# Kernel optimization log

Hardware: AMD Instinct MI355X
Metric: run time of the kernel (lower is better)

Reference implementation:

```python
import jax, jax.numpy as jnp
import numpy as np

B = 1
T_FRAMES = 512
LDIM = 512
D = 512
H = 8
DH = 64
L = 8
FF = 2048
CTX = 250
RATIOS = (8, 6, 5, 4)
MAX_PERIOD = 10000.0


def setup_inputs() -> dict:
    key = jax.random.key(0)
    ks = iter(jax.random.split(key, 80))
    def rn(shape, s=0.02):
        return jax.random.normal(next(ks), shape, jnp.float32) * s
    inp = {}
    inp['latent'] = rn((B, LDIM, T_FRAMES), 1.0)
    inp['emb_std'] = jax.random.uniform(next(ks), (LDIM,), jnp.float32, 0.5, 1.5)
    inp['emb_mean'] = rn((LDIM,), 0.1)
    inp['quant_w'] = rn((D, LDIM)); inp['quant_b'] = jnp.zeros((D,))
    inp['up_w'] = rn((D, D, 4)); inp['up_b'] = jnp.zeros((D,))
    inp['n1w'] = jnp.ones((L, D)); inp['n1b'] = jnp.zeros((L, D))
    inp['ipw'] = rn((L, 3 * D, D)); inp['ipb'] = jnp.zeros((L, 3 * D))
    inp['opw'] = rn((L, D, D)); inp['opb'] = jnp.zeros((L, D))
    inp['ls1'] = jnp.full((L, D), 0.01)
    inp['n2w'] = jnp.ones((L, D)); inp['n2b'] = jnp.zeros((L, D))
    inp['l1w'] = rn((L, FF, D)); inp['l1b'] = jnp.zeros((L, FF))
    inp['l2w'] = rn((L, D, FF)); inp['l2b'] = jnp.zeros((L, D))
    inp['ls2'] = jnp.full((L, D), 0.01)
    inp['tproj_w'] = rn((D, D)); inp['tproj_b'] = jnp.zeros((D,))
    inp['dc0_w'] = rn((1024, D, 7)); inp['dc0_b'] = jnp.zeros((1024,))
    ch = 1024
    for i, r in enumerate(RATIOS, 1):
        co = ch // 2
        inp['t%d_w' % i] = rn((ch, co, 2 * r)); inp['t%d_b' % i] = jnp.zeros((co,))
        inp['r%da_w' % i] = rn((co // 2, co, 3)); inp['r%da_b' % i] = jnp.zeros((co // 2,))
        inp['r%db_w' % i] = rn((co, co // 2, 1)); inp['r%db_b' % i] = jnp.zeros((co,))
        ch = co
    inp['df_w'] = rn((1, 64, 7)); inp['df_b'] = jnp.zeros((1,))
    return {k: jnp.asarray(v, jnp.float32) for k, v in inp.items()}


def _ln(x, w, b):
    m = x.mean(-1, keepdims=True)
    v = ((x - m) ** 2).mean(-1, keepdims=True)
    return (x - m) / jnp.sqrt(v + 1e-5) * w + b


def _rope(x, cos, sin):
    # x: (B,T,H,DH); cos/sin: (T,1,DH//2)
    b_, t_, h_, d_ = x.shape
    xr = x.reshape(b_, t_, h_, d_ // 2, 2)
    re, im = xr[..., 0], xr[..., 1]
    out = jnp.stack([re * cos - im * sin, re * sin + im * cos], axis=-1)
    return out.reshape(b_, t_, h_, d_)


def _conv(x, w, b, stride=1):
    # StreamingConv1d non-streaming: left-pad by k-stride (zeros), then valid conv.
    k = w.shape[-1]
    pad = k - stride
    if pad > 0:
        x = jnp.pad(x, ((0, 0), (0, 0), (pad, 0)))
    y = jax.lax.conv_general_dilated(x, w, (stride,), 'VALID',
                                     dimension_numbers=('NCH', 'OIH', 'NCH'))
    return y + b[None, :, None]


def _convtr(x, w, b, stride):
    # torch ConvTranspose1d, padding=0: w is (in, out, k); L_out=(L-1)*stride+k
    k = w.shape[-1]
    w2 = jnp.swapaxes(jnp.flip(w, -1), 0, 1)  # (out, in, k)
    y = jax.lax.conv_general_dilated(x, w2, (1,), [(k - 1, k - 1)],
                                     lhs_dilation=(stride,),
                                     dimension_numbers=('NCH', 'OIH', 'NCH'))
    return y + b[None, :, None]


def _forward(latent, emb_std, emb_mean, quant_w, quant_b, up_w, up_b,
             n1w, n1b, ipw, ipb, opw, opb, ls1, n2w, n2b, l1w, l1b, l2w, l2b, ls2,
             tproj_w, tproj_b, dc0_w, dc0_b,
             t1_w, t1_b, r1a_w, r1a_b, r1b_w, r1b_b,
             t2_w, t2_b, r2a_w, r2a_b, r2b_w, r2b_b,
             t3_w, t3_b, r3a_w, r3a_b, r3b_w, r3b_b,
             t4_w, t4_b, r4a_w, r4a_b, r4b_w, r4b_b,
             df_w, df_b):
    # denormalize + quantizer output proj (1x1 conv)
    x = latent * emb_std[None, :, None] + emb_mean[None, :, None]
    x = jnp.einsum('od,bdt->bot', quant_w, x) + quant_b[None, :, None]
    # upsample (raw convtr, no trimming)
    x = _convtr(x, up_w, up_b, 2)
    z = jnp.swapaxes(x, 1, 2)  # (B, T, D)
    T = z.shape[1]
    # windowed causal additive mask: attend to previous `CTX` positions incl. self
    pos = jnp.arange(T)
    delta = pos[:, None] - pos[None, :]
    mask = jnp.where((delta >= 0) & (delta < CTX), 0.0, -jnp.inf).astype(jnp.float32)
    # RoPE tables (offset = 0)
    fr = jnp.exp(jnp.arange(DH // 2, dtype=jnp.float32) * (-np.log(MAX_PERIOD) * 2.0 / DH))
    ang = jnp.arange(T, dtype=jnp.float32)[:, None, None] * fr  # (T,1,DH//2)
    cos, sin = jnp.cos(ang), jnp.sin(ang)
    scale = 1.0 / np.sqrt(DH)

    def step(h, p):
        n1w_, n1b_, ipw_, ipb_, opw_, opb_, ls1_, n2w_, n2b_, l1w_, l1b_, l2w_, l2b_, ls2_ = p
        hn = _ln(h, n1w_, n1b_)
        qkv = (jnp.einsum('btd,ed->bte', hn, ipw_) + ipb_).reshape(B, T, 3, H, DH)
        q, k, v = qkv[:, :, 0], qkv[:, :, 1], qkv[:, :, 2]
        q = _rope(q, cos, sin)
        k = _rope(k, cos, sin)
        s = jnp.einsum('bqhd,bkhd->bhqk', q, k) * scale + mask
        a = jax.nn.softmax(s, axis=-1)
        o = jnp.einsum('bhqk,bkhd->bqhd', a, v).reshape(B, T, D)
        o = jnp.einsum('btd,ed->bte', o, opw_) + opb_
        h = h + ls1_ * o
        hn2 = _ln(h, n2w_, n2b_)
        ff = jax.nn.gelu(jnp.einsum('btd,fd->btf', hn2, l1w_) + l1b_, approximate=False)
        ff = jnp.einsum('btf,df->btd', ff, l2w_) + l2b_
        h = h + ls2_ * ff
        return h, None

    z, _ = jax.lax.scan(step, z, (n1w, n1b, ipw, ipb, opw, opb, ls1,
                                  n2w, n2b, l1w, l1b, l2w, l2b, ls2))
    z = jnp.einsum('btd,ed->bte', z, tproj_w) + tproj_b
    z = jnp.swapaxes(z, 1, 2)  # (B, D, T)
    # SEANet decoder
    z = _conv(z, dc0_w, dc0_b, 1)
    stages = ((t1_w, t1_b, r1a_w, r1a_b, r1b_w, r1b_b, 8),
              (t2_w, t2_b, r2a_w, r2a_b, r2b_w, r2b_b, 6),
              (t3_w, t3_b, r3a_w, r3a_b, r3b_w, r3b_b, 5),
              (t4_w, t4_b, r4a_w, r4a_b, r4b_w, r4b_b, 4))
    for tw, tb, raw_, rab_, rbw_, rbb_, st in stages:
        z = jax.nn.elu(z)
        z = _convtr(z, tw, tb, st)
        v2 = _conv(jax.nn.elu(z), raw_, rab_, 1)
        v2 = _conv(jax.nn.elu(v2), rbw_, rbb_, 1)
        z = z + v2  # residual block skip
    z = jax.nn.elu(z)
    z = _conv(z, df_w, df_b, 1)
    return z  # (B, 1, T_samples)


def reference(latent, emb_std, emb_mean, quant_w, quant_b, up_w, up_b,
              n1w, n1b, ipw, ipb, opw, opb, ls1, n2w, n2b, l1w, l1b, l2w, l2b, ls2,
              tproj_w, tproj_b, dc0_w, dc0_b,
              t1_w, t1_b, r1a_w, r1a_b, r1b_w, r1b_b,
              t2_w, t2_b, r2a_w, r2a_b, r2b_w, r2b_b,
              t3_w, t3_b, r3a_w, r3a_b, r3b_w, r3b_b,
              t4_w, t4_b, r4a_w, r4a_b, r4b_w, r4b_b,
              df_w, df_b):
    return _forward(latent, emb_std, emb_mean, quant_w, quant_b, up_w, up_b,
                    n1w, n1b, ipw, ipb, opw, opb, ls1, n2w, n2b, l1w, l1b, l2w, l2b, ls2,
                    tproj_w, tproj_b, dc0_w, dc0_b,
                    t1_w, t1_b, r1a_w, r1a_b, r1b_w, r1b_b,
                    t2_w, t2_b, r2a_w, r2a_b, r2b_w, r2b_b,
                    t3_w, t3_b, r3a_w, r3a_b, r3b_w, r3b_b,
                    t4_w, t4_b, r4a_w, r4a_b, r4b_w, r4b_b,
                    df_w, df_b)
```

## Files before the change

kernel.cpp:

```cpp
#include <hip/hip_runtime.h>
#include <math.h>

typedef __attribute__((ext_vector_type(8))) short short8;
typedef __attribute__((ext_vector_type(4))) float f32x4;

#define MFMA16(a, b, c) __builtin_amdgcn_mfma_f32_16x16x32_bf16((a), (b), (c), 0, 0, 0)

__device__ __forceinline__ unsigned bfu(float f) {
    unsigned u = __float_as_uint(f);
    return (u + 0x7fffu + ((u >> 16) & 1u)) >> 16;
}

static constexpr int TT   = 1026;
static constexpr int T_S1 = 8216;
static constexpr int T_S2 = 49302;
static constexpr int T_S3 = 246515;
static constexpr int T_S4 = 986064;

static constexpr int NCH    = 8;
static constexpr int LC     = T_S4 / NCH;
static constexpr int LE_MAX = LC + 8;

static constexpr size_t O_X0  = 0;
static constexpr size_t O_XQ  = 262144;
static constexpr size_t O_XU  = 524288;
static constexpr size_t O_Z   = 1049600;
static constexpr size_t O_HN  = 1574912;
static constexpr size_t O_QKV = 2100224;
static constexpr size_t O_AO  = 3676160;
static constexpr size_t O_FF  = 4201472;
static constexpr size_t O_COS = 6302720;
static constexpr size_t O_SIN = 6335552;
static constexpr size_t O_ZT  = 6368384;
static constexpr size_t O_ZC  = 6893696;
static constexpr size_t O_D0  = 7419008;
static constexpr size_t O_Z1  = 8469632;
static constexpr size_t O_V1  = 12676224;
static constexpr size_t O_Z2  = 31553920;
static constexpr size_t O_V2  = 0;
static constexpr size_t O_Z3  = 0;
static constexpr size_t O_V3  = 31553920;
static constexpr size_t O_Z4C = 31553920;
static constexpr size_t O_VAC = 39442944;

static inline int cdiv(int a, int b) { return (a + b - 1) / b; }

__global__ __launch_bounds__(256) void embed_k(const float* __restrict__ lat,
    const float* __restrict__ sd, const float* __restrict__ mn, float* __restrict__ y)
{
    int i = blockIdx.x * 256 + threadIdx.x;
    if (i >= 512 * 512) return;
    int c = i >> 9;
    y[i] = lat[i] * sd[c] + mn[c];
}

__global__ __launch_bounds__(256) void rope_tables(float* __restrict__ cs, float* __restrict__ sn)
{
    int idx = blockIdx.x * 256 + threadIdx.x;
    if (idx >= TT * 32) return;
    int i = idx & 31;
    int t = idx >> 5;
    float fr = expf(-(float)i * (logf(10000.f) / 32.f));
    float ang = (float)t * fr;
    cs[idx] = cosf(ang);
    sn[idx] = sinf(ang);
}

__global__ __launch_bounds__(256) void rope_apply(float* __restrict__ qkv,
    const float* __restrict__ cs, const float* __restrict__ sn)
{
    int idx = blockIdx.x * 256 + threadIdx.x;
    if (idx >= TT * 8 * 32) return;
    int i = idx & 31;
    int h = (idx >> 5) & 7;
    int t = idx >> 8;
    float c = cs[t * 32 + i], s = sn[t * 32 + i];
    size_t base = (size_t)t * 1536 + h * 64 + 2 * i;
    float re = qkv[base], im = qkv[base + 1];
    qkv[base]     = re * c - im * s;
    qkv[base + 1] = re * s + im * c;
    base += 512;
    re = qkv[base]; im = qkv[base + 1];
    qkv[base]     = re * c - im * s;
    qkv[base + 1] = re * s + im * c;
}

__global__ __launch_bounds__(256) void transpose_k(const float* __restrict__ in,
    float* __restrict__ out, int R, int C)
{
    __shared__ float tile[32][33];
    int c0 = blockIdx.x * 32, r0 = blockIdx.y * 32;
    int tx = threadIdx.x & 31, ty = threadIdx.x >> 5;
    for (int dy = ty; dy < 32; dy += 8) {
        int r = r0 + dy, c = c0 + tx;
        tile[dy][tx] = (r < R && c < C) ? in[(size_t)r * C + c] : 0.f;
    }
    __syncthreads();
    for (int dy = ty; dy < 32; dy += 8) {
        int c = c0 + dy, r = r0 + tx;
        if (c < C && r < R) out[(size_t)c * R + r] = tile[tx][dy];
    }
}

__global__ __launch_bounds__(256) void ln_kernel(const float* __restrict__ x,
    const float* __restrict__ w, const float* __restrict__ b, float* __restrict__ y)
{
    int t = blockIdx.x, tid = threadIdx.x;
    const float* xr = x + (size_t)t * 512;
    float v0 = xr[tid], v1 = xr[tid + 256];
    float s = v0 + v1, q = v0 * v0 + v1 * v1;
    for (int off = 32; off; off >>= 1) {
        s += __shfl_down(s, off);
        q += __shfl_down(q, off);
    }
    __shared__ float ss[4], qq[4], mb[2];
    int wid = tid >> 6, lane = tid & 63;
    if (lane == 0) { ss[wid] = s; qq[wid] = q; }
    __syncthreads();
    if (tid == 0) {
        float S = ss[0] + ss[1] + ss[2] + ss[3];
        float Q = qq[0] + qq[1] + qq[2] + qq[3];
        float m = S * (1.f / 512.f);
        float var = Q * (1.f / 512.f) - m * m;
        mb[0] = m;
        mb[1] = rsqrtf(var + 1e-5f);
    }
    __syncthreads();
    float m = mb[0], inv = mb[1];
    y[(size_t)t * 512 + tid]       = (v0 - m) * inv * w[tid] + b[tid];
    y[(size_t)t * 512 + tid + 256] = (v1 - m) * inv * w[tid + 256] + b[tid + 256];
}

__global__ __launch_bounds__(256) void attn_kernel(const float* __restrict__ qkv,
    float* __restrict__ o)
{
    int t = blockIdx.x, h = blockIdx.y, tid = threadIdx.x;
    __shared__ float sq[64];
    __shared__ float sp[256];
    __shared__ float red[256];
    __shared__ float pacc[4][64];
    int klo = t - 249; if (klo < 0) klo = 0;
    int kc = t - klo + 1;
    if (tid < 64) sq[tid] = qkv[(size_t)t * 1536 + h * 64 + tid];
    __syncthreads();
    float sval = -3.0e38f;
    if (tid < kc) {
        const float* kr = qkv + (size_t)(klo + tid) * 1536 + 512 + h * 64;
        float d = 0.f;
#pragma unroll 8
        for (int i = 0; i < 64; i++) d += sq[i] * kr[i];
        sval = d * 0.125f;
    }
    red[tid] = sval;
    __syncthreads();
    for (int s2 = 128; s2 > 0; s2 >>= 1) {
        if (tid < s2) red[tid] = fmaxf(red[tid], red[tid + s2]);
        __syncthreads();
    }
    float m = red[0];
    __syncthreads();
    float p = (tid < kc) ? __expf(sval - m) : 0.f;
    sp[tid] = p;
    red[tid] = p;
    __syncthreads();
    for (int s2 = 128; s2 > 0; s2 >>= 1) {
        if (tid < s2) red[tid] += red[tid + s2];
        __syncthreads();
    }
    float inv = 1.f / red[0];
    int d = tid & 63, g = tid >> 6;
    float a = 0.f;
#pragma unroll 4
    for (int kk = g; kk < kc; kk += 4)
        a += sp[kk] * qkv[(size_t)(klo + kk) * 1536 + 1024 + h * 64 + d];
    pacc[g][d] = a;
    __syncthreads();
    if (tid < 64) {
        float r = (pacc[0][tid] + pacc[1][tid] + pacc[2][tid] + pacc[3][tid]) * inv;
        o[(size_t)t * 512 + h * 64 + tid] = r;
    }
}

template <int EPI>
__global__ __launch_bounds__(256, 3) void mfma_gemm(const float* __restrict__ A,
    const float* __restrict__ Wt, const float* __restrict__ bias,
    const float* __restrict__ ls, float* __restrict__ C, int M, int N, int K)
{
    constexpr int STR = 72;
    __shared__ unsigned short sA[128 * STR];
    __shared__ unsigned short sB[128 * STR];
    int tid = threadIdx.x;
    int m0 = blockIdx.y * 128, n0 = blockIdx.x * 128;
    int w = tid >> 6, lane = tid & 63;
    int wm = (w >> 1) * 64, wn = (w & 1) * 64;
    int row15 = lane & 15, q8 = (lane >> 4) * 8;
    int rb = tid >> 3;
    int sg = (tid & 7) * 8;
    f32x4 acc[4][4] = {};
    float4 av[8], bv[8];
    const float4 z4 = make_float4(0.f, 0.f, 0.f, 0.f);
    for (int k0 = 0; k0 < K; k0 += 64) {
#pragma unroll
        for (int it = 0; it < 4; it++) {
            int r = rb + it * 32;
            int gm = m0 + r;
            if (gm < M) {
                const float4* p = (const float4*)(A + (size_t)gm * K + k0 + sg);
                av[2 * it] = p[0]; av[2 * it + 1] = p[1];
            } else { av[2 * it] = z4; av[2 * it + 1] = z4; }
            int gn = n0 + r;
            if (gn < N) {
                const float4* p = (const float4*)(Wt + (size_t)gn * K + k0 + sg);
                bv[2 * it] = p[0]; bv[2 * it + 1] = p[1];
            } else { bv[2 * it] = z4; bv[2 * it + 1] = z4; }
        }
        __syncthreads();
#pragma unroll
        for (int it = 0; it < 4; it++) {
            int r = rb + it * 32;
            unsigned* d = (unsigned*)&sA[r * STR + sg];
            float4 f0 = av[2 * it], f1 = av[2 * it + 1];
            d[0] = bfu(f0.x) | (bfu(f0.y) << 16); d[1] = bfu(f0.z) | (bfu(f0.w) << 16);
            d[2] = bfu(f1.x) | (bfu(f1.y) << 16); d[3] = bfu(f1.z) | (bfu(f1.w) << 16);
            d = (unsigned*)&sB[r * STR + sg];
            f0 = bv[2 * it]; f1 = bv[2 * it + 1];
            d[0] = bfu(f0.x) | (bfu(f0.y) << 16); d[1] = bfu(f0.z) | (bfu(f0.w) << 16);
            d[2] = bfu(f1.x) | (bfu(f1.y) << 16); d[3] = bfu(f1.z) | (bfu(f1.w) << 16);
        }
        __syncthreads();
#pragma unroll
        for (int kk = 0; kk < 64; kk += 32) {
            short8 af[4], bf[4];
#pragma unroll
            for (int f = 0; f < 4; f++) {
                af[f] = *(const short8*)&sA[(wm + f * 16 + row15) * STR + kk + q8];
                bf[f] = *(const short8*)&sB[(wn + f * 16 + row15) * STR + kk + q8];
            }
#pragma unroll
            for (int i = 0; i < 4; i++)
#pragma unroll
                for (int j = 0; j < 4; j++)
                    acc[i][j] = MFMA16(af[i], bf[j], acc[i][j]);
        }
    }
    int rq = (lane >> 4) * 4;
#pragma unroll
    for (int i = 0; i < 4; i++) {
#pragma unroll
        for (int r = 0; r < 4; r++) {
            int m = m0 + wm + i * 16 + rq + r;
            if (m >= M) continue;
#pragma unroll
            for (int j = 0; j < 4; j++) {
                int n = n0 + wn + j * 16 + row15;
                float v = acc[i][j][r] + bias[n];
                size_t idx = (size_t)m * N + n;
                if (EPI == 0) C[idx] = v;
                else if (EPI == 1) C[idx] = 0.5f * v * (1.f + erff(v * 0.70710678118654752f));
                else C[idx] += ls[n] * v;
            }
        }
    }
}

template <int K, bool ELU_IN, bool ACC>
__global__ __launch_bounds__(256, 3) void mfma_conv(
    const float* __restrict__ x, const float* __restrict__ w,
    const float* __restrict__ bias, float* __restrict__ y,
    int Ci, int Co, int x_str, int Tx, int x_t0, int Ty, int y_t0, int to_lo, int to_hi)
{
    constexpr int TL = 128 + K - 1;
    constexpr int SX = 40;
    constexpr int SW = 40;
    constexpr int NX = (32 * TL + 255) / 256;
    constexpr int NWK = 8 * K;
    __shared__ unsigned short sX[TL * SX];
    __shared__ unsigned short sW[K * 64 * SW];
    int tid = threadIdx.x;
    int co0 = blockIdx.y * 64;
    int t_base = to_lo + blockIdx.x * 128;
    int w_id = tid >> 6, lane = tid & 63;
    int wm = (w_id >> 1) * 32, wn = (w_id & 1) * 64;
    int row15 = lane & 15, q8 = (lane >> 4) * 8;
    f32x4 acc[2][4] = {};
    float xv[NX], wv[NWK];
    for (int ci0 = 0; ci0 < Ci; ci0 += 32) {
#pragma unroll
        for (int it = 0; it < NX; it++) {
            int i = tid + it * 256;
            float v = 0.f;
            if (i < 32 * TL) {
                int ci = i / TL, tl = i - ci * TL;
                int gl = t_base - (K - 1) + tl - x_t0;
                if (gl >= 0 && gl < Tx) v = x[(size_t)(ci0 + ci) * x_str + gl];
            }
            xv[it] = v;
        }
#pragma unroll
        for (int it = 0; it < NWK; it++) {
            int i = tid + it * 256;
            int co = i / (32 * K), r = i - co * (32 * K);
            int ci = r / K, j = r - ci * K;
            wv[it] = (co0 + co < Co)
                ? w[((size_t)(co0 + co) * Ci + ci0 + ci) * K + j] : 0.f;
        }
        __syncthreads();
#pragma unroll
        for (int it = 0; it < NX; it++) {
            int i = tid + it * 256;
            if (i < 32 * TL) {
                int ci = i / TL, tl = i - ci * TL;
                float v = xv[it];
                if (ELU_IN) v = v > 0.f ? v : __expf(v) - 1.f;
                sX[tl * SX + ci] = (unsigned short)bfu(v);
            }
        }
#pragma unroll
        for (int it = 0; it < NWK; it++) {
            int i = tid + it * 256;
            int co = i / (32 * K), r = i - co * (32 * K);
            int ci = r / K, j = r - ci * K;
            sW[(j * 64 + co) * SW + ci] = (unsigned short)bfu(wv[it]);
        }
        __syncthreads();
#pragma unroll
        for (int j = 0; j < K; j++) {
            short8 af[2], bf[4];
#pragma unroll
            for (int f = 0; f < 2; f++)
                af[f] = *(const short8*)&sW[(j * 64 + wm + f * 16 + row15) * SW + q8];
#pragma unroll
            for (int f = 0; f < 4; f++)
                bf[f] = *(const short8*)&sX[(wn + f * 16 + row15 + j) * SX + q8];
#pragma unroll
            for (int i = 0; i < 2; i++)
#pragma unroll
                for (int f = 0; f < 4; f++)
                    acc[i][f] = MFMA16(af[i], bf[f], acc[i][f]);
        }
    }
    int rq = (lane >> 4) * 4;
#pragma unroll
    for (int i = 0; i < 2; i++) {
#pragma unroll
        for (int r = 0; r < 4; r++) {
            int co = co0 + wm + i * 16 + rq + r;
            if (co >= Co) continue;
            float b = bias[co];
#pragma unroll
            for (int f = 0; f < 4; f++) {
                int t = t_base + wn + f * 16 + row15;
                if (t < to_hi) {
                    size_t idx = (size_t)co * Ty + (t - y_t0);
                    float v = acc[i][f][r] + b;
                    if (ACC) y[idx] += v; else y[idx] = v;
                }
            }
        }
    }
}

template <int S, int PG, bool ELU_IN>
__global__ __launch_bounds__(256, 3) void mfma_convtr(
    const float* __restrict__ x, const float* __restrict__ w,
    const float* __restrict__ bias, float* __restrict__ y,
    int Ci, int Co, int Ti, int Ty, int y_t0, int q_lo, int to_lo, int to_hi)
{
    constexpr int SX = 40;
    constexpr int SW = 40;
    constexpr int NW = PG * 2;
    __shared__ unsigned short sX[256 * SX];
    __shared__ unsigned short sW[PG * 16 * SW];
    int tid = threadIdx.x;
    int co0 = blockIdx.y * 16;
    int q0 = q_lo + blockIdx.x * 256;
    int p0 = blockIdx.z * PG;
    int w_id = tid >> 6, lane = tid & 63;
    int row15 = lane & 15, q8 = (lane >> 4) * 8;
    f32x4 acc[PG][4] = {};
    int q = q0 + tid;
    bool qok0 = (q >= 0) && (q < Ti);
    bool qok1 = (q >= 1) && (q <= Ti);
    float xv0[16], xv1[16], wv[NW];

    auto prefetch = [&](int ci0) {
#pragma unroll
        for (int it = 0; it < 16; it++) {
            const float* xr = x + (size_t)(ci0 + it) * Ti;
            xv0[it] = qok0 ? xr[q] : 0.f;
            xv1[it] = qok1 ? xr[q - 1] : 0.f;
        }
#pragma unroll
        for (int it = 0; it < NW; it++) {
            int i = tid + it * 256;
            int pl = i >> 9, r = i & 511;
            int co = r >> 5, k = r & 31;
            int ci = k >> 1, tap = k & 1;
            wv[it] = (p0 + pl < S)
                ? w[((size_t)(ci0 + ci) * Co + co0 + co) * (2 * S) + tap * S + p0 + pl]
                : 0.f;
        }
    };
    auto commit = [&]() {
#pragma unroll
        for (int it = 0; it < 16; it++) {
            float v0 = xv0[it], v1 = xv1[it];
            if (ELU_IN) {
                v0 = v0 > 0.f ? v0 : __expf(v0) - 1.f;
                v1 = v1 > 0.f ? v1 : __expf(v1) - 1.f;
            }
            *(unsigned*)&sX[tid * SX + 2 * it] = bfu(v0) | (bfu(v1) << 16);
        }
#pragma unroll
        for (int it = 0; it < NW; it++) {
            int i = tid + it * 256;
            int pl = i >> 9, r = i & 511;
            int co = r >> 5, k = r & 31;
            sW[(pl * 16 + co) * SW + k] = (unsigned short)bfu(wv[it]);
        }
    };

    prefetch(0);
    for (int ci0 = 0; ci0 < Ci; ci0 += 16) {
        __syncthreads();
        commit();
        if (ci0 + 16 < Ci) prefetch(ci0 + 16);
        __syncthreads();
        short8 bf[4];
#pragma unroll
        for (int f = 0; f < 4; f++)
            bf[f] = *(const short8*)&sX[(w_id * 64 + f * 16 + row15) * SX + q8];
#pragma unroll
        for (int p = 0; p < PG; p++) {
            short8 af = *(const short8*)&sW[(p * 16 + row15) * SW + q8];
#pragma unroll
            for (int f = 0; f < 4; f++)
                acc[p][f] = MFMA16(af, bf[f], acc[p][f]);
        }
    }
    int rq = (lane >> 4) * 4;
#pragma unroll
    for (int r = 0; r < 4; r++) {
        int co = co0 + rq + r;
        float b = bias[co];
#pragma unroll
        for (int f = 0; f < 4; f++) {
            int qq = q0 + w_id * 64 + f * 16 + row15;
#pragma unroll
            for (int p = 0; p < PG; p++) {
                int to = qq * S + p0 + p;
                if (to >= to_lo && to < to_hi)
                    y[(size_t)co * Ty + (to - y_t0)] = acc[p][f][r] + b;
            }
        }
    }
}

__global__ __launch_bounds__(256) void conv7_out_chunk(const float* __restrict__ z4c,
    const float* __restrict__ w, const float* __restrict__ bias,
    float* __restrict__ out, int ext0, int t0, int cnt)
{
    __shared__ float ws_w[64 * 7];
    int tl = blockIdx.x * 256 + threadIdx.x;
    for (int i = threadIdx.x; i < 448; i += 256) ws_w[i] = w[i];
    __syncthreads();
    if (tl >= cnt) return;
    int t = t0 + tl;
    float acc = bias[0];
    for (int ci = 0; ci < 64; ci++) {
        const float* xr = z4c + (size_t)ci * LE_MAX;
#pragma unroll
        for (int j = 0; j < 7; j++) {
            int tg = t - 6 + j;
            float v = 0.f;
            if (tg >= 0) {
                float z = xr[tg - ext0];
                v = z > 0.f ? z : __expf(z) - 1.f;
            }
            acc += ws_w[ci * 7 + j] * v;
        }
    }
    out[t] = acc;
}

template <int K, bool ELU_IN, bool ACC>
static void conv_launch(const float* x, const float* w, const float* b, float* y,
    int Ci, int Co, int x_str, int Tx, int x_t0, int Ty, int y_t0, int to_lo, int to_hi,
    hipStream_t stream)
{
    dim3 g(cdiv(to_hi - to_lo, 128), cdiv(Co, 64));
    mfma_conv<K, ELU_IN, ACC><<<g, 256, 0, stream>>>(x, w, b, y, Ci, Co, x_str, Tx, x_t0, Ty, y_t0, to_lo, to_hi);
}

template <int S, int PG, bool ELU_IN>
static void convtr_launch(const float* x, const float* w, const float* b, float* y,
    int Ci, int Co, int Ti, int Ty, int y_t0, int to_lo, int to_hi, hipStream_t stream)
{
    int q_lo = to_lo / S;
    int q_hi = (to_hi - 1) / S;
    dim3 g(cdiv(q_hi - q_lo + 1, 256), Co / 16, cdiv(S, PG));
    mfma_convtr<S, PG, ELU_IN><<<g, 256, 0, stream>>>(x, w, b, y, Ci, Co, Ti, Ty, y_t0, q_lo, to_lo, to_hi);
}

extern "C" void kernel_launch(void* const* d_in, const int* in_sizes, int n_in,
                              void* d_out, int out_size, void* d_ws, size_t ws_size,
                              hipStream_t stream)
{
    const float* latent  = (const float*)d_in[0];
    const float* emb_std = (const float*)d_in[1];
    const float* emb_mean= (const float*)d_in[2];
    const float* quant_w = (const float*)d_in[3];
    const float* quant_b = (const float*)d_in[4];
    const float* up_w    = (const float*)d_in[5];
    const float* up_b    = (const float*)d_in[6];
    const float* n1w     = (const float*)d_in[7];
    const float* n1b     = (const float*)d_in[8];
    const float* ipw     = (const float*)d_in[9];
    const float* ipb     = (const float*)d_in[10];
    const float* opw     = (const float*)d_in[11];
    const float* opb     = (const float*)d_in[12];
    const float* ls1     = (const float*)d_in[13];
    const float* n2w     = (const float*)d_in[14];
    const float* n2b     = (const float*)d_in[15];
    const float* l1w     = (const float*)d_in[16];
    const float* l1b     = (const float*)d_in[17];
    const float* l2w     = (const float*)d_in[18];
    const float* l2b     = (const float*)d_in[19];
    const float* ls2     = (const float*)d_in[20];
    const float* tproj_w = (const float*)d_in[21];
    const float* tproj_b = (const float*)d_in[22];
    const float* dc0_w   = (const float*)d_in[23];
    const float* dc0_b   = (const float*)d_in[24];
    const float* df_w    = (const float*)d_in[49];
    const float* df_b    = (const float*)d_in[50];

    float* W = (float*)d_ws;
    float* OUT = (float*)d_out;

    embed_k<<<cdiv(512 * 512, 256), 256, 0, stream>>>(latent, emb_std, emb_mean, W + O_X0);
    conv_launch<1, false, false>(W + O_X0, quant_w, quant_b, W + O_XQ,
        512, 512, 512, 512, 0, 512, 0, 0, 512, stream);
    convtr_launch<2, 2, false>(W + O_XQ, up_w, up_b, W + O_XU,
        512, 512, 512, TT, 0, 0, TT, stream);
    transpose_k<<<dim3(cdiv(TT, 32), cdiv(512, 32)), 256, 0, stream>>>(W + O_XU, W + O_Z, 512, TT);
    rope_tables<<<cdiv(TT * 32, 256), 256, 0, stream>>>(W + O_COS, W + O_SIN);

    for (int l = 0; l < 8; l++) {
        ln_kernel<<<TT, 256, 0, stream>>>(W + O_Z, n1w + l * 512, n1b + l * 512, W + O_HN);
        mfma_gemm<0><<<dim3(1536 / 128, cdiv(TT, 128)), 256, 0, stream>>>(
            W + O_HN, ipw + (size_t)l * 1536 * 512, ipb + l * 1536, nullptr, W + O_QKV, TT, 1536, 512);
        rope_apply<<<cdiv(TT * 8 * 32, 256), 256, 0, stream>>>(W + O_QKV, W + O_COS, W + O_SIN);
        attn_kernel<<<dim3(TT, 8), 256, 0, stream>>>(W + O_QKV, W + O_AO);
        mfma_gemm<2><<<dim3(512 / 128, cdiv(TT, 128)), 256, 0, stream>>>(
            W + O_AO, opw + (size_t)l * 512 * 512, opb + l * 512, ls1 + l * 512, W + O_Z, TT, 512, 512);
        ln_kernel<<<TT, 256, 0, stream>>>(W + O_Z, n2w + l * 512, n2b + l * 512, W + O_HN);
        mfma_gemm<1><<<dim3(2048 / 128, cdiv(TT, 128)), 256, 0, stream>>>(
            W + O_HN, l1w + (size_t)l * 2048 * 512, l1b + l * 2048, nullptr, W + O_FF, TT, 2048, 512);
        mfma_gemm<2><<<dim3(512 / 128, cdiv(TT, 128)), 256, 0, stream>>>(
            W + O_FF, l2w + (size_t)l * 512 * 2048, l2b + l * 512, ls2 + l * 512, W + O_Z, TT, 512, 2048);
    }

    mfma_gemm<0><<<dim3(512 / 128, cdiv(TT, 128)), 256, 0, stream>>>(
        W + O_Z, tproj_w, tproj_b, nullptr, W + O_ZT, TT, 512, 512);
    transpose_k<<<dim3(cdiv(512, 32), cdiv(TT, 32)), 256, 0, stream>>>(W + O_ZT, W + O_ZC, TT, 512);
    conv_launch<7, false, false>(W + O_ZC, dc0_w, dc0_b, W + O_D0,
        512, 1024, TT, TT, 0, TT, 0, 0, TT, stream);

    {
        const float* tw = (const float*)d_in[25]; const float* tb = (const float*)d_in[26];
        const float* raw = (const float*)d_in[27]; const float* rab = (const float*)d_in[28];
        const float* rbw = (const float*)d_in[29]; const float* rbb = (const float*)d_in[30];
        convtr_launch<8, 4, true>(W + O_D0, tw, tb, W + O_Z1,
            1024, 512, TT, T_S1, 0, 0, T_S1, stream);
        conv_launch<3, true, false>(W + O_Z1, raw, rab, W + O_V1,
            512, 256, T_S1, T_S1, 0, T_S1, 0, 0, T_S1, stream);
        conv_launch<1, true, true>(W + O_V1, rbw, rbb, W + O_Z1,
            256, 512, T_S1, T_S1, 0, T_S1, 0, 0, T_S1, stream);
    }
    {
        const float* tw = (const float*)d_in[31]; const float* tb = (const float*)d_in[32];
        const float* raw = (const float*)d_in[33]; const float* rab = (const float*)d_in[34];
        const float* rbw = (const float*)d_in[35]; const float* rbb = (const float*)d_in[36];
        convtr_launch<6, 3, true>(W + O_Z1, tw, tb, W + O_Z2,
            512, 256, T_S1, T_S2, 0, 0, T_S2, stream);
        conv_launch<3, true, false>(W + O_Z2, raw, rab, W + O_V2,
            256, 128, T_S2, T_S2, 0, T_S2, 0, 0, T_S2, stream);
        conv_launch<1, true, true>(W + O_V2, rbw, rbb, W + O_Z2,
            128, 256, T_S2, T_S2, 0, T_S2, 0, 0, T_S2, stream);
    }
    {
        const float* tw = (const float*)d_in[37]; const float* tb = (const float*)d_in[38];
        const float* raw = (const float*)d_in[39]; const float* rab = (const float*)d_in[40];
        const float* rbw = (const float*)d_in[41]; const float* rbb = (const float*)d_in[42];
        convtr_launch<5, 5, true>(W + O_Z2, tw, tb, W + O_Z3,
            256, 128, T_S2, T_S3, 0, 0, T_S3, stream);
        conv_launch<3, true, false>(W + O_Z3, raw, rab, W + O_V3,
            128, 64, T_S3, T_S3, 0, T_S3, 0, 0, T_S3, stream);
        conv_launch<1, true, true>(W + O_V3, rbw, rbb, W + O_Z3,
            64, 128, T_S3, T_S3, 0, T_S3, 0, 0, T_S3, stream);
    }
    {
        const float* tw = (const float*)d_in[43]; const float* tb = (const float*)d_in[44];
        const float* raw = (const float*)d_in[45]; const float* rab = (const float*)d_in[46];
        const float* rbw = (const float*)d_in[47]; const float* rbb = (const float*)d_in[48];
        for (int c = 0; c < NCH; c++) {
            int t0 = c * LC;
            int ext0 = (c == 0) ? 0 : t0 - 8;
            int Le = t0 + LC - ext0;
            int vlo = (c == 0) ? 0 : ext0 + 2;
            convtr_launch<4, 4, true>(W + O_Z3, tw, tb, W + O_Z4C,
                128, 64, T_S3, LE_MAX, ext0, ext0, ext0 + Le, stream);
            conv_launch<3, true, false>(W + O_Z4C, raw, rab, W + O_VAC,
                64, 32, LE_MAX, Le, ext0, LE_MAX, ext0, vlo, ext0 + Le, stream);
            conv_launch<1, true, true>(W + O_VAC, rbw, rbb, W + O_Z4C,
                32, 64, LE_MAX, Le, ext0, LE_MAX, ext0, vlo, ext0 + Le, stream);
            conv7_out_chunk<<<dim3(cdiv(LC, 256), 1), 256, 0, stream>>>(
                W + O_Z4C, df_w, df_b, OUT, ext0, t0, LC);
        }
    }
}
```

Measured before the change: 5.857 ms.

## Split-K with atomics for small convs, add prefetch pipelining and block swizzle

Adds a split-K mode over input channels to the conv and transposed-conv kernels. Partial sums are combined with atomicAdd into zero-filled outputs, which gives the small early layers enough blocks to fill the GPU. It also adds register prefetch of the next K-tile in the GEMM and conv loops, vectorised float4 weight loads in the conv, and a block-index swizzle meant to improve cache locality. The costs are extra zero-fill launches, atomic traffic, and non-deterministic float summation order.

```diff
diff --git a/kernel.cpp b/kernel.cpp
--- a/kernel.cpp
+++ b/kernel.cpp
@@ -9,6 +9,17 @@
 __device__ __forceinline__ unsigned bfu(float f) {
     unsigned u = __float_as_uint(f);
     return (u + 0x7fffu + ((u >> 16) & 1u)) >> 16;
+}
+
+__device__ __forceinline__ void swz_block(unsigned& bx, unsigned& by, unsigned& bz) {
+    unsigned gx = gridDim.x, gy = gridDim.y, gz = gridDim.z;
+    unsigned nb = gx * gy * gz;
+    unsigned d = blockIdx.x + gx * (blockIdx.y + gy * blockIdx.z);
+    if ((nb & 7u) == 0u) d = (d & 7u) * (nb >> 3) + (d >> 3);
+    bx = d % gx;
+    unsigned r = d / gx;
+    by = r % gy;
+    bz = r / gy;
 }
 
 static constexpr int TT   = 1026;
@@ -45,6 +56,18 @@
 
 static inline int cdiv(int a, int b) { return (a + b - 1) / b; }
 
+__global__ __launch_bounds__(256) void fill0(float4* __restrict__ p, int n4)
+{
+    int i = blockIdx.x * 256 + threadIdx.x;
+    if (i < n4) p[i] = make_float4(0.f, 0.f, 0.f, 0.f);
+}
+
+static void zero_launch(float* p, size_t n, hipStream_t s)
+{
+    int n4 = (int)(n / 4);
+    fill0<<<cdiv(n4, 256), 256, 0, s>>>((float4*)p, n4);
+}
+
 __global__ __launch_bounds__(256) void embed_k(const float* __restrict__ lat,
     const float* __restrict__ sd, const float* __restrict__ mn, float* __restrict__ y)
 {
@@ -190,7 +213,8 @@
     __shared__ unsigned short sA[128 * STR];
     __shared__ unsigned short sB[128 * STR];
     int tid = threadIdx.x;
-    int m0 = blockIdx.y * 128, n0 = blockIdx.x * 128;
+    unsigned bxs, bys, bzs; swz_block(bxs, bys, bzs);
+    int m0 = bys * 128, n0 = bxs * 128;
     int w = tid >> 6, lane = tid & 63;
     int wm = (w >> 1) * 64, wn = (w & 1) * 64;
     int row15 = lane & 15, q8 = (lane >> 4) * 8;
@@ -199,7 +223,8 @@
     f32x4 acc[4][4] = {};
     float4 av[8], bv[8];
     const float4 z4 = make_float4(0.f, 0.f, 0.f, 0.f);
-    for (int k0 = 0; k0 < K; k0 += 64) {
+
+    auto prefetch = [&](int k0) {
 #pragma unroll
         for (int it = 0; it < 4; it++) {
             int r = rb + it * 32;
@@ -214,6 +239,10 @@
                 bv[2 * it] = p[0]; bv[2 * it + 1] = p[1];
             } else { bv[2 * it] = z4; bv[2 * it + 1] = z4; }
         }
+    };
+
+    prefetch(0);
+    for (int k0 = 0; k0 < K; k0 += 64) {
         __syncthreads();
 #pragma unroll
         for (int it = 0; it < 4; it++) {
@@ -228,6 +257,7 @@
             d[2] = bfu(f1.x) | (bfu(f1.y) << 16); d[3] = bfu(f1.z) | (bfu(f1.w) << 16);
         }
         __syncthreads();
+        if (k0 + 64 < K) prefetch(k0 + 64);
 #pragma unroll
         for (int kk = 0; kk < 64; kk += 32) {
             short8 af[4], bf[4];
@@ -263,28 +293,35 @@
     }
 }
 
-template <int K, bool ELU_IN, bool ACC>
+template <int K, bool ELU_IN, bool ACC, bool ATOM>
 __global__ __launch_bounds__(256, 3) void mfma_conv(
     const float* __restrict__ x, const float* __restrict__ w,
     const float* __restrict__ bias, float* __restrict__ y,
-    int Ci, int Co, int x_str, int Tx, int x_t0, int Ty, int y_t0, int to_lo, int to_hi)
+    int Ci, int Co, int x_str, int Tx, int x_t0, int Ty, int y_t0, int to_lo, int to_hi,
+    int nz)
 {
     constexpr int TL = 128 + K - 1;
     constexpr int SX = 40;
     constexpr int SW = 40;
     constexpr int NX = (32 * TL + 255) / 256;
-    constexpr int NWK = 8 * K;
+    constexpr int NW4 = 2 * K;
     __shared__ unsigned short sX[TL * SX];
     __shared__ unsigned short sW[K * 64 * SW];
     int tid = threadIdx.x;
-    int co0 = blockIdx.y * 64;
-    int t_base = to_lo + blockIdx.x * 128;
+    unsigned bxs, bys, bzs; swz_block(bxs, bys, bzs);
+    int co0 = bys * 64;
+    int t_base = to_lo + bxs * 128;
+    int cpz = (Ci / 32) / nz;
+    int ci_b = (int)bzs * cpz * 32, ci_e = ci_b + cpz * 32;
     int w_id = tid >> 6, lane = tid & 63;
     int wm = (w_id >> 1) * 32, wn = (w_id & 1) * 64;
     int row15 = lane & 15, q8 = (lane >> 4) * 8;
     f32x4 acc[2][4] = {};
-    float xv[NX], wv[NWK];
-    for (int ci0 = 0; ci0 < Ci; ci0 += 32) {
+    float xv[NX];
+    float4 wv4[NW4];
+    const float4 z4 = make_float4(0.f, 0.f, 0.f, 0.f);
+
+    auto prefetch = [&](int ci0) {
 #pragma unroll
         for (int it = 0; it < NX; it++) {
             int i = tid + it * 256;
@@ -297,14 +334,15 @@
             xv[it] = v;
         }
 #pragma unroll
-        for (int it = 0; it < NWK; it++) {
-            int i = tid + it * 256;
-            int co = i / (32 * K), r = i - co * (32 * K);
-            int ci = r / K, j = r - ci * K;
-            wv[it] = (co0 + co < Co)
-                ? w[((size_t)(co0 + co) * Ci + ci0 + ci) * K + j] : 0.f;
-        }
-        __syncthreads();
+        for (int it = 0; it < NW4; it++) {
+            int i4 = tid + it * 256;
+            int co = i4 / (8 * K), r4 = i4 - co * (8 * K);
+            wv4[it] = (co0 + co < Co)
+                ? *(const float4*)(w + ((size_t)(co0 + co) * Ci + ci0) * K + r4 * 4)
+                : z4;
+        }
+    };
+    auto commit = [&]() {
 #pragma unroll
         for (int it = 0; it < NX; it++) {
             int i = tid + it * 256;
@@ -316,13 +354,26 @@
             }
         }
 #pragma unroll
-        for (int it = 0; it < NWK; it++) {
-            int i = tid + it * 256;
-            int co = i / (32 * K), r = i - co * (32 * K);
-            int ci = r / K, j = r - ci * K;
-            sW[(j * 64 + co) * SW + ci] = (unsigned short)bfu(wv[it]);
-        }
-        __syncthreads();
+        for (int it = 0; it < NW4; it++) {
+            int i4 = tid + it * 256;
+            int co = i4 / (8 * K), r4 = i4 - co * (8 * K);
+            float4 f = wv4[it];
+#pragma unroll
+            for (int e = 0; e < 4; e++) {
+                int k = r4 * 4 + e;
+                int ci = k / K, j = k - ci * K;
+                float fv = (e == 0) ? f.x : (e == 1) ? f.y : (e == 2) ? f.z : f.w;
+                sW[(j * 64 + co) * SW + ci] = (unsigned short)bfu(fv);
+            }
+        }
+    };
+
+    prefetch(ci_b);
+    for (int ci0 = ci_b; ci0 < ci_e; ci0 += 32) {
+        __syncthreads();
+        commit();
+        __syncthreads();
+        if (ci0 + 32 < ci_e) prefetch(ci0 + 32);
 #pragma unroll
         for (int j = 0; j < K; j++) {
             short8 af[2], bf[4];
@@ -346,25 +397,28 @@
         for (int r = 0; r < 4; r++) {
             int co = co0 + wm + i * 16 + rq + r;
             if (co >= Co) continue;
-            float b = bias[co];
+            float b = (!ATOM || bzs == 0) ? bias[co] : 0.f;
 #pragma unroll
             for (int f = 0; f < 4; f++) {
                 int t = t_base + wn + f * 16 + row15;
                 if (t < to_hi) {
                     size_t idx = (size_t)co * Ty + (t - y_t0);
                     float v = acc[i][f][r] + b;
-                    if (ACC) y[idx] += v; else y[idx] = v;
+                    if (ATOM) atomicAdd(&y[idx], v);
+                    else if (ACC) y[idx] += v;
+                    else y[idx] = v;
                 }
             }
         }
     }
 }
 
-template <int S, int PG, bool ELU_IN>
+template <int S, int PG, bool ELU_IN, bool ATOM>
 __global__ __launch_bounds__(256, 3) void mfma_convtr(
     const float* __restrict__ x, const float* __restrict__ w,
     const float* __restrict__ bias, float* __restrict__ y,
-    int Ci, int Co, int Ti, int Ty, int y_t0, int q_lo, int to_lo, int to_hi)
+    int Ci, int Co, int Ti, int Ty, int y_t0, int q_lo, int to_lo, int to_hi,
+    int nPG, int nz)
 {
     constexpr int SX = 40;
     constexpr int SW = 40;
@@ -372,9 +426,13 @@
     __shared__ unsigned short sX[256 * SX];
     __shared__ unsigned short sW[PG * 16 * SW];
     int tid = threadIdx.x;
-    int co0 = blockIdx.y * 16;
-    int q0 = q_lo + blockIdx.x * 256;
-    int p0 = blockIdx.z * PG;
+    unsigned bxs, bys, bzs; swz_block(bxs, bys, bzs);
+    int co0 = bys * 16;
+    int q0 = q_lo + (int)bxs * 256;
+    int pgi = (int)bzs % nPG, zi = (int)bzs / nPG;
+    int p0 = pgi * PG;
+    int cpz = (Ci / 16) / nz;
+    int ci_b = zi * cpz * 16, ci_e = ci_b + cpz * 16;
     int w_id = tid >> 6, lane = tid & 63;
     int row15 = lane & 15, q8 = (lane >> 4) * 8;
     f32x4 acc[PG][4] = {};
@@ -420,12 +478,12 @@
         }
     };
 
-    prefetch(0);
-    for (int ci0 = 0; ci0 < Ci; ci0 += 16) {
+    prefetch(ci_b);
+    for (int ci0 = ci_b; ci0 < ci_e; ci0 += 16) {
         __syncthreads();
         commit();
-        if (ci0 + 16 < Ci) prefetch(ci0 + 16);
-        __syncthreads();
+        __syncthreads();
+        if (ci0 + 16 < ci_e) prefetch(ci0 + 16);
         short8 bf[4];
 #pragma unroll
         for (int f = 0; f < 4; f++)
@@ -442,15 +500,19 @@
 #pragma unroll
     for (int r = 0; r < 4; r++) {
         int co = co0 + rq + r;
-        float b = bias[co];
+        float b = (!ATOM || zi == 0) ? bias[co] : 0.f;
 #pragma unroll
         for (int f = 0; f < 4; f++) {
             int qq = q0 + w_id * 64 + f * 16 + row15;
 #pragma unroll
             for (int p = 0; p < PG; p++) {
                 int to = qq * S + p0 + p;
-                if (to >= to_lo && to < to_hi)
-                    y[(size_t)co * Ty + (to - y_t0)] = acc[p][f][r] + b;
+                if (to >= to_lo && to < to_hi) {
+                    size_t idx = (size_t)co * Ty + (to - y_t0);
+                    float v = acc[p][f][r] + b;
+                    if (ATOM) atomicAdd(&y[idx], v);
+                    else y[idx] = v;
+                }
             }
         }
     }
@@ -483,23 +545,24 @@
     out[t] = acc;
 }
 
-template <int K, bool ELU_IN, bool ACC>
+template <int K, bool ELU_IN, bool ACC, bool ATOM>
 static void conv_launch(const float* x, const float* w, const float* b, float* y,
     int Ci, int Co, int x_str, int Tx, int x_t0, int Ty, int y_t0, int to_lo, int to_hi,
-    hipStream_t stream)
-{
-    dim3 g(cdiv(to_hi - to_lo, 128), cdiv(Co, 64));
-    mfma_conv<K, ELU_IN, ACC><<<g, 256, 0, stream>>>(x, w, b, y, Ci, Co, x_str, Tx, x_t0, Ty, y_t0, to_lo, to_hi);
-}
-
-template <int S, int PG, bool ELU_IN>
+    int nz, hipStream_t stream)
+{
+    dim3 g(cdiv(to_hi - to_lo, 128), cdiv(Co, 64), nz);
+    mfma_conv<K, ELU_IN, ACC, ATOM><<<g, 256, 0, stream>>>(x, w, b, y, Ci, Co, x_str, Tx, x_t0, Ty, y_t0, to_lo, to_hi, nz);
+}
+
+template <int S, int PG, bool ELU_IN, bool ATOM>
 static void convtr_launch(const float* x, const float* w, const float* b, float* y,
-    int Ci, int Co, int Ti, int Ty, int y_t0, int to_lo, int to_hi, hipStream_t stream)
+    int Ci, int Co, int Ti, int Ty, int y_t0, int to_lo, int to_hi, int nz, hipStream_t stream)
 {
     int q_lo = to_lo / S;
     int q_hi = (to_hi - 1) / S;
-    dim3 g(cdiv(q_hi - q_lo + 1, 256), Co / 16, cdiv(S, PG));
-    mfma_convtr<S, PG, ELU_IN><<<g, 256, 0, stream>>>(x, w, b, y, Ci, Co, Ti, Ty, y_t0, q_lo, to_lo, to_hi);
+    int nPG = cdiv(S, PG);
+    dim3 g(cdiv(q_hi - q_lo + 1, 256), Co / 16, nPG * nz);
+    mfma_convtr<S, PG, ELU_IN, ATOM><<<g, 256, 0, stream>>>(x, w, b, y, Ci, Co, Ti, Ty, y_t0, q_lo, to_lo, to_hi, nPG, nz);
 }
 
 extern "C" void kernel_launch(void* const* d_in, const int* in_sizes, int n_in,
@@ -538,10 +601,12 @@
     float* OUT = (float*)d_out;
 
     embed_k<<<cdiv(512 * 512, 256), 256, 0, stream>>>(latent, emb_std, emb_mean, W + O_X0);
-    conv_launch<1, false, false>(W + O_X0, quant_w, quant_b, W + O_XQ,
-        512, 512, 512, 512, 0, 512, 0, 0, 512, stream);
-    convtr_launch<2, 2, false>(W + O_XQ, up_w, up_b, W + O_XU,
-        512, 512, 512, TT, 0, 0, TT, stream);
+    zero_launch(W + O_XQ, (size_t)512 * 512, stream);
+    conv_launch<1, false, false, true>(W + O_X0, quant_w, quant_b, W + O_XQ,
+        512, 512, 512, 512, 0, 512, 0, 0, 512, 8, stream);
+    zero_launch(W + O_XU, (size_t)512 * TT, stream);
+    convtr_launch<2, 2, false, true>(W + O_XQ, up_w, up_b, W + O_XU,
+        512, 512, 512, TT, 0, 0, TT, 8, stream);
     transpose_k<<<dim3(cdiv(TT, 32), cdiv(512, 32)), 256, 0, stream>>>(W + O_XU, W + O_Z, 512, TT);
     rope_tables<<<cdiv(TT * 32, 256), 256, 0, stream>>>(W + O_COS, W + O_SIN);
 
@@ -563,41 +628,44 @@
     mfma_gemm<0><<<dim3(512 / 128, cdiv(TT, 128)), 256, 0, stream>>>(
         W + O_Z, tproj_w, tproj_b, nullptr, W + O_ZT, TT, 512, 512);
     transpose_k<<<dim3(cdiv(512, 32), cdiv(TT, 32)), 256, 0, stream>>>(W + O_ZT, W + O_ZC, TT, 512);
-    conv_launch<7, false, false>(W + O_ZC, dc0_w, dc0_b, W + O_D0,
-        512, 1024, TT, TT, 0, TT, 0, 0, TT, stream);
+    zero_launch(W + O_D0, (size_t)1024 * TT, stream);
+    conv_launch<7, false, false, true>(W + O_ZC, dc0_w, dc0_b, W + O_D0,
+        512, 1024, TT, TT, 0, TT, 0, 0, TT, 4, stream);
 
     {
         const float* tw = (const float*)d_in[25]; const float* tb = (const float*)d_in[26];
         const float* raw = (const float*)d_in[27]; const float* rab = (const float*)d_in[28];
         const float* rbw = (const float*)d_in[29]; const float* rbb = (const float*)d_in[30];
-        convtr_launch<8, 4, true>(W + O_D0, tw, tb, W + O_Z1,
-            1024, 512, TT, T_S1, 0, 0, T_S1, stream);
-        conv_launch<3, true, false>(W + O_Z1, raw, rab, W + O_V1,
-            512, 256, T_S1, T_S1, 0, T_S1, 0, 0, T_S1, stream);
-        conv_launch<1, true, true>(W + O_V1, rbw, rbb, W + O_Z1,
-            256, 512, T_S1, T_S1, 0, T_S1, 0, 0, T_S1, stream);
+        zero_launch(W + O_Z1, (size_t)512 * T_S1, stream);
+        convtr_launch<8, 4, true, true>(W + O_D0, tw, tb, W + O_Z1,
+            1024, 512, TT, T_S1, 0, 0, T_S1, 4, stream);
+        zero_launch(W + O_V1, (size_t)256 * T_S1, stream);
+        conv_launch<3, true, false, true>(W + O_Z1, raw, rab, W + O_V1,
+            512, 256, T_S1, T_S1, 0, T_S1, 0, 0, T_S1, 4, stream);
+        conv_launch<1, true, true, true>(W + O_V1, rbw, rbb, W + O_Z1,
+            256, 512, T_S1, T_S1, 0, T_S1, 0, 0, T_S1, 2, stream);
     }
     {
         const float* tw = (const float*)d_in[31]; const float* tb = (const float*)d_in[32];
         const float* raw = (const float*)d_in[33]; const float* rab = (const float*)d_in[34];
         const float* rbw = (const float*)d_in[35]; const float* rbb = (const float*)d_in[36];
-        convtr_launch<6, 3, true>(W + O_Z1, tw, tb, W + O_Z2,
-            512, 256, T_S1, T_S2, 0, 0, T_S2, stream);
-        conv_launch<3, true, false>(W + O_Z2, raw, rab, W + O_V2,
-            256, 128, T_S2, T_S2, 0, T_S2, 0, 0, T_S2, stream);
-        conv_launch<1, true, true>(W + O_V2, rbw, rbb, W + O_Z2,
-            128, 256, T_S2, T_S2, 0, T_S2, 0, 0, T_S2, stream);
+        convtr_launch<6, 3, true, false>(W + O_Z1, tw, tb, W + O_Z2,
+            512, 256, T_S1, T_S2, 0, 0, T_S2, 1, stream);
+        conv_launch<3, true, false, false>(W + O_Z2, raw, rab, W + O_V2,
+            256, 128, T_S2, T_S2, 0, T_S2, 0, 0, T_S2, 1, stream);
+        conv_launch<1, true, true, false>(W + O_V2, rbw, rbb, W + O_Z2,
+            128, 256, T_S2, T_S2, 0, T_S2, 0, 0, T_S2, 1, stream);
     }
     {
         const float* tw = (const float*)d_in[37]; const float* tb = (const float*)d_in[38];
         const float* raw = (const float*)d_in[39]; const float* rab = (const float*)d_in[40];
         const float* rbw = (const float*)d_in[41]; const float* rbb = (const float*)d_in[42];
-        convtr_launch<5, 5, true>(W + O_Z2, tw, tb, W + O_Z3,
-            256, 128, T_S2, T_S3, 0, 0, T_S3, stream);
-        conv_launch<3, true, false>(W + O_Z3, raw, rab, W + O_V3,
-            128, 64, T_S3, T_S3, 0, T_S3, 0, 0, T_S3, stream);
-        conv_launch<1, true, true>(W + O_V3, rbw, rbb, W + O_Z3,
-            64, 128, T_S3, T_S3, 0, T_S3, 0, 0, T_S3, stream);
+        convtr_launch<5, 5, true, false>(W + O_Z2, tw, tb, W + O_Z3,
+            256, 128, T_S2, T_S3, 0, 0, T_S3, 1, stream);
+        conv_launch<3, true, false, false>(W + O_Z3, raw, rab, W + O_V3,
+            128, 64, T_S3, T_S3, 0, T_S3, 0, 0, T_S3, 1, stream);
+        conv_launch<1, true, true, false>(W + O_V3, rbw, rbb, W + O_Z3,
+            64, 128, T_S3, T_S3, 0, T_S3, 0, 0, T_S3, 1, stream);
     }
     {
         const float* tw = (const float*)d_in[43]; const float* tb = (const float*)d_in[44];
@@ -608,12 +676,12 @@
             int ext0 = (c == 0) ? 0 : t0 - 8;
             int Le = t0 + LC - ext0;
             int vlo = (c == 0) ? 0 : ext0 + 2;
-            convtr_launch<4, 4, true>(W + O_Z3, tw, tb, W + O_Z4C,
-                128, 64, T_S3, LE_MAX, ext0, ext0, ext0 + Le, stream);
-            conv_launch<3, true, false>(W + O_Z4C, raw, rab, W + O_VAC,
-                64, 32, LE_MAX, Le, ext0, LE_MAX, ext0, vlo, ext0 + Le, stream);
-            conv_launch<1, true, true>(W + O_VAC, rbw, rbb, W + O_Z4C,
-                32, 64, LE_MAX, Le, ext0, LE_MAX, ext0, vlo, ext0 + Le, stream);
+            convtr_launch<4, 4, true, false>(W + O_Z3, tw, tb, W + O_Z4C,
+                128, 64, T_S3, LE_MAX, ext0, ext0, ext0 + Le, 1, stream);
+            conv_launch<3, true, false, false>(W + O_Z4C, raw, rab, W + O_VAC,
+                64, 32, LE_MAX, Le, ext0, LE_MAX, ext0, vlo, ext0 + Le, 1, stream);
+            conv_launch<1, true, true, false>(W + O_VAC, rbw, rbb, W + O_Z4C,
+                32, 64, LE_MAX, Le, ext0, LE_MAX, ext0, vlo, ext0 + Le, 1, stream);
             conv7_out_chunk<<<dim3(cdiv(LC, 256), 1), 256, 0, stream>>>(
                 W + O_Z4C, df_w, df_b, OUT, ext0, t0, LC);
         }
```

After: 7.385 ms. 1.26x slower.
